# Kernel optimization log

Measured on AMD Instinct MI355X. Metric: run time of the kernel, lower is better.

The kernel has to match this reference:

```python
import jax, jax.numpy as jnp
import numpy as np
import math

H = 8  # num_heads
SCALE = 1.0 / math.sqrt(512.0)  # original divides by sqrt(dim_V), not sqrt(head_dim)


def setup_inputs() -> dict:
    key = jax.random.key(0)
    ks = jax.random.split(key, 16)
    B, N, D = 32, 512, 512
    s = 1.0 / math.sqrt(D)
    return {
        "Q": jax.random.normal(ks[0], (B, N, D), jnp.float32),
        "K": jax.random.normal(ks[1], (B, N, D), jnp.float32),
        "Wq": jax.random.normal(ks[2], (D, D), jnp.float32) * s,
        "bq": jnp.zeros((D,), jnp.float32),
        "Wk": jax.random.normal(ks[3], (D, D), jnp.float32) * s,
        "bk": jnp.zeros((D,), jnp.float32),
        "Wv": jax.random.normal(ks[4], (D, D), jnp.float32) * s,
        "bv": jnp.zeros((D,), jnp.float32),
        "Wo": jax.random.normal(ks[5], (D, D), jnp.float32) * s,
        "bo": jnp.zeros((D,), jnp.float32),
        "W1": jax.random.normal(ks[6], (D, D), jnp.float32) * s,
        "b1": jnp.zeros((D,), jnp.float32),
        "W2": jax.random.normal(ks[7], (D, D), jnp.float32) * s,
        "b2": jnp.zeros((D,), jnp.float32),
    }


def reference(Q, K, Wq, bq, Wk, bk, Wv, bv, Wo, bo, W1, b1, W2, b2):
    B, Nq, D = Q.shape
    dh = D // H
    # projections (torch Linear: x @ W.T + b)
    q = (Q @ Wq.T + bq).reshape(B, Nq, H, dh)
    k = (K @ Wk.T + bk).reshape(B, K.shape[1], H, dh)
    v = (K @ Wv.T + bv).reshape(B, K.shape[1], H, dh)
    # scores: [B, H, Nq, Nk], scaled by 1/sqrt(dim_V)
    scores = jnp.einsum("bqhd,bkhd->bhqk", q, k) * SCALE
    # NOTE: original softmax is over dim=1 of [H*B, Nq, Nk] == the QUERY axis
    A = jax.nn.softmax(scores, axis=2)
    attn = jnp.einsum("bhqk,bkhd->bqhd", A, v).reshape(B, Nq, D)
    out = Q + (attn @ Wo.T + bo)  # dropout p=0.0
    ffn = jax.nn.relu(out @ W1.T + b1) @ W2.T + b2
    return out + ffn
```

## Files before the change

### kernel.cpp

```cpp
#include <hip/hip_runtime.h>
#include <stdint.h>

#define SCALE_ 0.044194173824159216f
#define QSC_ (0.044194173824159216f * 1.4426950408889634f)

typedef __attribute__((ext_vector_type(8))) short bf16x8;
typedef __attribute__((ext_vector_type(4))) float f32x4;
typedef __attribute__((ext_vector_type(16))) float f32x16;
typedef __attribute__((ext_vector_type(2))) unsigned int uint2v;

__device__ __forceinline__ ushort f2b(float f) {
  union { float f; uint32_t u; } v; v.f = f;
  return (ushort)((v.u + 0x7fffu + ((v.u >> 16) & 1u)) >> 16);
}
__device__ __forceinline__ uint32_t cvtpk(float lo, float hi) {
  uint32_t r; asm("v_cvt_pk_bf16_f32 %0, %1, %2" : "=v"(r) : "v"(lo), "v"(hi)); return r;
}
__device__ __forceinline__ float ex2(float x) {
  float r; asm("v_exp_f32 %0, %1" : "=v"(r) : "v"(x)); return r;
}
__device__ __forceinline__ void gld16(void* lds, const void* g) {
  __builtin_amdgcn_global_load_lds(
      (const __attribute__((address_space(1))) uint32_t*)g,
      (__attribute__((address_space(3))) uint32_t*)lds, 16, 0, 0);
}

__global__ __launch_bounds__(256)
void k_cvtw(const float* __restrict__ w0, const float* __restrict__ w1,
            const float* __restrict__ w2, const float* __restrict__ w3,
            const float* __restrict__ w4, const float* __restrict__ w5,
            ushort* __restrict__ Wb)
{
  const int NW = 262144;
  int i = (blockIdx.x * 256 + threadIdx.x) * 4;
  int seg = i >> 18;
  int off = i & (NW - 1);
  const float* src;
  switch (seg) { case 0: src = w0; break; case 1: src = w1; break; case 2: src = w2; break;
                 case 3: src = w3; break; case 4: src = w4; break; default: src = w5; }
  float4 v = *(const float4*)(src + off);
  ushort4 o = make_ushort4(f2b(v.x), f2b(v.y), f2b(v.z), f2b(v.w));
  *(ushort4*)(Wb + (size_t)seg * NW + off) = o;
}

template<int EPI>
__device__ __forceinline__ void gemm_body(const ushort* __restrict__ A, const ushort* __restrict__ Bw,
                                          const float* __restrict__ bias, const float* __restrict__ extra,
                                          float* __restrict__ outf, ushort* __restrict__ outb,
                                          char* lds, int m0, int n0)
{
  const int t = threadIdx.x;
  const int w = t >> 6, lane = t & 63;
  const int wm = w >> 1, wn = w & 1;
  const int rA = lane & 15, g = lane >> 4;

  const ushort* srcA[4]; int ldsA[4];
#pragma unroll
  for (int j = 0; j < 4; j++) {
    int L = (t + j*512) * 16;
    int U = L ^ (((L >> 7) & 7) << 4);
    srcA[j] = A + (size_t)(m0 + (U >> 7))*512 + ((U & 127) >> 1);
    ldsA[j] = L;
  }
  const ushort* srcB[2]; int ldsB[2];
#pragma unroll
  for (int j = 0; j < 2; j++) {
    int L = (t + j*512) * 16;
    int U = L ^ (((L >> 7) & 7) << 4);
    srcB[j] = Bw + (size_t)(n0 + (U >> 7))*512 + ((U & 127) >> 1);
    ldsB[j] = 32768 + L;
  }

#define STAGE_A(ti) do { char* bb_ = lds + ((ti) % 3) * 49152; \
    _Pragma("unroll") \
    for (int j = 0; j < 4; j++) gld16(bb_ + ldsA[j], srcA[j] + (ti)*64); } while (0)
#define STAGE_B(ti) do { char* bb_ = lds + ((ti) % 3) * 49152; \
    _Pragma("unroll") \
    for (int j = 0; j < 2; j++) gld16(bb_ + ldsB[j], srcB[j] + (ti)*64); } while (0)

  STAGE_A(0); STAGE_B(0);
  STAGE_A(1); STAGE_B(1);

  f32x4 acc[4][4] = {};
  for (int i = 0; i < 8; i++) {
    if (i < 7) asm volatile("s_waitcnt vmcnt(6)" ::: "memory");
    else       asm volatile("s_waitcnt vmcnt(0)" ::: "memory");
    __builtin_amdgcn_s_barrier();
    __builtin_amdgcn_sched_barrier(0);
    const char* bufc = lds + (i % 3) * 49152;

    bf16x8 afA[4], bfA[4], afB[4], bfB[4];
#pragma unroll
    for (int m = 0; m < 4; m++) {
      int row = wm*64 + m*16 + rA;
      afA[m] = *(const bf16x8*)(bufc + ((row*128 + g*16) ^ ((row & 7) << 4)));
      afB[m] = *(const bf16x8*)(bufc + ((row*128 + 64 + g*16) ^ ((row & 7) << 4)));
    }
#pragma unroll
    for (int n = 0; n < 4; n++) {
      int row = wn*64 + n*16 + rA;
      bfA[n] = *(const bf16x8*)(bufc + 32768 + ((row*128 + g*16) ^ ((row & 7) << 4)));
      bfB[n] = *(const bf16x8*)(bufc + 32768 + ((row*128 + 64 + g*16) ^ ((row & 7) << 4)));
    }
    if (i < 6) { STAGE_A(i + 2); STAGE_B(i + 2); }
    __builtin_amdgcn_sched_barrier(0);
    __builtin_amdgcn_s_setprio(1);
#pragma unroll
    for (int m = 0; m < 4; m++)
#pragma unroll
      for (int n = 0; n < 4; n++)
        acc[m][n] = __builtin_amdgcn_mfma_f32_16x16x32_bf16(afA[m], bfA[n], acc[m][n], 0, 0, 0);
#pragma unroll
    for (int m = 0; m < 4; m++)
#pragma unroll
      for (int n = 0; n < 4; n++)
        acc[m][n] = __builtin_amdgcn_mfma_f32_16x16x32_bf16(afB[m], bfB[n], acc[m][n], 0, 0, 0);
    __builtin_amdgcn_s_setprio(0);
  }
#undef STAGE_A
#undef STAGE_B

#pragma unroll
  for (int m = 0; m < 4; m++)
#pragma unroll
    for (int n = 0; n < 4; n++) {
      int col = n0 + wn*64 + n*16 + rA;
      float bb = bias[col];
#pragma unroll
      for (int r = 0; r < 4; r++) {
        int row = m0 + wm*64 + m*16 + g*4 + r;
        size_t idx = (size_t)row*512 + col;
        float v = acc[m][n][r] + bb;
        if (EPI == 1)      { float o = extra[idx] + v; outf[idx] = o; outb[idx] = f2b(o); }
        else if (EPI == 2) outb[idx] = f2b(v > 0.f ? v : 0.f);
        else               outf[idx] += v;
      }
    }
}

template<int EPI>
__global__ __launch_bounds__(512, 2)
void k_gemm(const ushort* __restrict__ A, const ushort* __restrict__ Bw,
            const float* __restrict__ bias, const float* __restrict__ extra,
            float* __restrict__ outf, ushort* __restrict__ outb)
{
  __shared__ __align__(16) char lds[3*49152];
  gemm_body<EPI>(A, Bw, bias, extra, outf, outb, lds, blockIdx.x*256, blockIdx.y*128);
}

template<int EPI>
__device__ __forceinline__ void gemm_f32a_body(const float* __restrict__ A32, const ushort* __restrict__ Bw,
                                               const float* __restrict__ bias,
                                               float* __restrict__ outf, ushort* __restrict__ outb,
                                               char* lds, int m0, int n0, float os)
{
  const int t = threadIdx.x;
  const int w = t >> 6, lane = t & 63;
  const int wm = w >> 1, wn = w & 1;
  const int rA = lane & 15, g = lane >> 4;

  const float* srcA[4]; int ldsA[4];
#pragma unroll
  for (int j = 0; j < 4; j++) {
    int L = (t + j*512) * 16;
    int U = L ^ (((L >> 7) & 7) << 4);
    srcA[j] = A32 + (size_t)(m0 + (U >> 7))*512 + ((U & 127) >> 1);
    ldsA[j] = L;
  }
  const ushort* srcB[2]; int ldsB[2];
#pragma unroll
  for (int j = 0; j < 2; j++) {
    int L = (t + j*512) * 16;
    int U = L ^ (((L >> 7) & 7) << 4);
    srcB[j] = Bw + (size_t)(n0 + (U >> 7))*512 + ((U & 127) >> 1);
    ldsB[j] = 32768 + L;
  }

#define QLA(ti, R) do { \
    _Pragma("unroll") \
    for (int j = 0; j < 4; j++) { \
      R[2*j]   = *(const float4*)(srcA[j] + (ti)*64); \
      R[2*j+1] = *(const float4*)(srcA[j] + (ti)*64 + 4); } } while (0)
#define QWA(ti, R) do { char* bb_ = lds + ((ti) % 3) * 49152; \
    _Pragma("unroll") \
    for (int j = 0; j < 4; j++) { \
      uint4 qq; \
      qq.x = cvtpk(R[2*j].x,   R[2*j].y); \
      qq.y = cvtpk(R[2*j].z,   R[2*j].w); \
      qq.z = cvtpk(R[2*j+1].x, R[2*j+1].y); \
      qq.w = cvtpk(R[2*j+1].z, R[2*j+1].w); \
      *(uint4*)(bb_ + ldsA[j]) = qq; } } while (0)
#define QSB(ti) do { char* bb_ = lds + ((ti) % 3) * 49152; \
    _Pragma("unroll") \
    for (int j = 0; j < 2; j++) gld16(bb_ + ldsB[j], srcB[j] + (ti)*64); } while (0)

  float4 a0[8], a1[8];
  QLA(0, a0);
  __builtin_amdgcn_sched_barrier(0);
  QLA(1, a1);
  __builtin_amdgcn_sched_barrier(0);
  QSB(0); QSB(1);
  __builtin_amdgcn_sched_barrier(0);
  asm volatile("s_waitcnt vmcnt(12)" ::: "memory");
  QWA(0, a0);

  f32x4 acc[4][4] = {};

#define QITER(i, RI, RW) do { \
    if ((i) == 0)      asm volatile("s_waitcnt vmcnt(2) lgkmcnt(0)" ::: "memory"); \
    else if ((i) == 7) asm volatile("s_waitcnt vmcnt(0) lgkmcnt(0)" ::: "memory"); \
    else               asm volatile("s_waitcnt vmcnt(10) lgkmcnt(0)" ::: "memory"); \
    __builtin_amdgcn_s_barrier(); \
    __builtin_amdgcn_sched_barrier(0); \
    const char* bufc = lds + ((i) % 3) * 49152; \
    bf16x8 afA[4], bfA[4], afB[4], bfB[4]; \
    _Pragma("unroll") \
    for (int m = 0; m < 4; m++) { \
      int row = wm*64 + m*16 + rA; \
      afA[m] = *(const bf16x8*)(bufc + ((row*128 + g*16) ^ ((row & 7) << 4))); \
      afB[m] = *(const bf16x8*)(bufc + ((row*128 + 64 + g*16) ^ ((row & 7) << 4))); \
    } \
    _Pragma("unroll") \
    for (int n = 0; n < 4; n++) { \
      int row = wn*64 + n*16 + rA; \
      bfA[n] = *(const bf16x8*)(bufc + 32768 + ((row*128 + g*16) ^ ((row & 7) << 4))); \
      bfB[n] = *(const bf16x8*)(bufc + 32768 + ((row*128 + 64 + g*16) ^ ((row & 7) << 4))); \
    } \
    if ((i) < 6) QLA((i) + 2, RI); \
    __builtin_amdgcn_sched_barrier(0); \
    if ((i) < 7) QWA((i) + 1, RW); \
    if ((i) < 6) QSB((i) + 2); \
    __builtin_amdgcn_sched_barrier(0); \
    __builtin_amdgcn_s_setprio(1); \
    _Pragma("unroll") \
    for (int m = 0; m < 4; m++) \
      _Pragma("unroll") \
      for (int n = 0; n < 4; n++) \
        acc[m][n] = __builtin_amdgcn_mfma_f32_16x16x32_bf16(afA[m], bfA[n], acc[m][n], 0, 0, 0); \
    _Pragma("unroll") \
    for (int m = 0; m < 4; m++) \
      _Pragma("unroll") \
      for (int n = 0; n < 4; n++) \
        acc[m][n] = __builtin_amdgcn_mfma_f32_16x16x32_bf16(afB[m], bfB[n], acc[m][n], 0, 0, 0); \
    __builtin_amdgcn_s_setprio(0); \
  } while (0)

  QITER(0, a0, a1);
  QITER(1, a1, a0);
  QITER(2, a0, a1);
  QITER(3, a1, a0);
  QITER(4, a0, a1);
  QITER(5, a1, a0);
  QITER(6, a0, a1);
  QITER(7, a1, a0);
#undef QITER
#undef QLA
#undef QWA
#undef QSB

#pragma unroll
  for (int m = 0; m < 4; m++)
#pragma unroll
    for (int n = 0; n < 4; n++) {
      int col = n0 + wn*64 + n*16 + rA;
      float bb = bias[col];
      if (EPI == 4) {
        int b = m0 >> 9, k0 = m0 & 511;
        int hh = col >> 6, dl = col & 63;
        int kg = k0 + wm*64 + m*16 + g*4;
        float v0 = acc[m][n][0] + bb, v1 = acc[m][n][1] + bb;
        float v2 = acc[m][n][2] + bb, v3 = acc[m][n][3] + bb;
        uint2 pk;
        pk.x = (uint32_t)f2b(v0) | ((uint32_t)f2b(v1) << 16);
        pk.y = (uint32_t)f2b(v2) | ((uint32_t)f2b(v3) << 16);
        *(uint2*)(outb + ((size_t)((b*8 + hh)*64 + dl)*512 + kg)) = pk;
      } else {
#pragma unroll
        for (int r = 0; r < 4; r++) {
          int row = m0 + wm*64 + m*16 + g*4 + r;
          size_t idx = (size_t)row*512 + col;
          outb[idx] = f2b((acc[m][n][r] + bb) * os);
        }
      }
    }
}

__global__ __launch_bounds__(512, 2)
void k_gemm_qkvf(const float* __restrict__ Qf, const float* __restrict__ Kf,
                 const ushort* __restrict__ Wb, const float* __restrict__ bq,
                 const float* __restrict__ bk, const float* __restrict__ bvv,
                 ushort* __restrict__ qkout, ushort* __restrict__ vpT)
{
  __shared__ __align__(16) char lds[3*49152];
  int z = blockIdx.z;
  if (z == 2) {
    gemm_f32a_body<4>(Kf, Wb + 2*(size_t)262144, bvv, nullptr, vpT,
                      lds, blockIdx.x*256, blockIdx.y*128, 1.0f);
  } else if (z == 1) {
    gemm_f32a_body<0>(Kf, Wb + (size_t)262144, bk, nullptr, qkout + (size_t)8388608,
                      lds, blockIdx.x*256, blockIdx.y*128, 1.0f);
  } else {
    gemm_f32a_body<0>(Qf, Wb, bq, nullptr, qkout,
                      lds, blockIdx.x*256, blockIdx.y*128, QSC_);
  }
}

__global__ __launch_bounds__(512, 2)
void k_att2(const ushort* __restrict__ qp, const ushort* __restrict__ kp,
            const ushort* __restrict__ vpT, float* __restrict__ zinv,
            ushort* __restrict__ attn)
{
  __shared__ __align__(16) char kt[65536];
  __shared__ __align__(16) char vt[65536];
  __shared__ __align__(16) char qpr[32768];
  int bh = blockIdx.x;
  int b = bh >> 3, h = bh & 7;
  int t = threadIdx.x, w = t >> 6, lane = t & 63;
  int rA = lane & 15, g = lane >> 4;
  const ushort* kbase = kp + (size_t)(b*512)*512 + h*64;
  const ushort* qbase = qp + (size_t)(b*512)*512 + h*64;
  const ushort* vbase = vpT + (size_t)bh*64*512;

#pragma unroll
  for (int i = 0; i < 8; i++) {
    int c = i*512 + t; int row = c >> 3, sl = c & 7;
    gld16(kt + c*16, kbase + (size_t)row*512 + ((sl ^ (row & 7))*8));
  }
#define STAGE_Q(buf, qb) do { \
    _Pragma("unroll") \
    for (int i = 0; i < 2; i++) { \
      int c = i*512 + t; int row = c >> 3, sl = c & 7; \
      gld16(qpr + (buf)*16384 + c*16, \
            qbase + (size_t)((qb)*128 + row)*512 + ((sl ^ (row & 7))*8)); } } while (0)
  STAGE_Q(0, 0);
  STAGE_Q(1, 1);
#pragma unroll
  for (int i = 0; i < 8; i++) {
    int c = i*512 + t; int d = c >> 6, sl = c & 63;
    gld16(vt + c*16, vbase + (size_t)d*512 + ((sl ^ (d & 7))*8));
  }

  asm volatile("s_waitcnt vmcnt(10)" ::: "memory");
  __builtin_amdgcn_s_barrier();
  __builtin_amdgcn_sched_barrier(0);
  bf16x8 kf[4][2];
#pragma unroll
  for (int n = 0; n < 4; n++)
#pragma unroll
    for (int ks = 0; ks < 2; ks++) {
      int k = w*64 + n*16 + rA;
      kf[n][ks] = *(const bf16x8*)(kt + k*128 + (((ks*4 + g) ^ (k & 7))*16));
    }
  float Zacc[4] = {0.f, 0.f, 0.f, 0.f};
  for (int qb = 0; qb < 4; qb++) {
    if (qb == 1)      { asm volatile("s_waitcnt vmcnt(10)" ::: "memory"); }
    else if (qb == 2) { asm volatile("s_waitcnt vmcnt(2)" ::: "memory"); }
    else if (qb == 3) { asm volatile("s_waitcnt vmcnt(0)" ::: "memory"); }
    if (qb) { __builtin_amdgcn_s_barrier(); __builtin_amdgcn_sched_barrier(0); }
    const char* qtb = qpr + (qb & 1)*16384;
    f32x4 acc[8][4] = {};
#pragma unroll
    for (int ks = 0; ks < 2; ks++) {
      bf16x8 af[8];
#pragma unroll
      for (int m = 0; m < 8; m++) {
        int q = m*16 + rA;
        af[m] = *(const bf16x8*)(qtb + q*128 + (((ks*4 + g) ^ (q & 7))*16));
      }
      __builtin_amdgcn_s_setprio(1);
#pragma unroll
      for (int m = 0; m < 8; m++)
#pragma unroll
        for (int n = 0; n < 4; n++)
          acc[m][n] = __builtin_amdgcn_mfma_f32_16x16x32_bf16(af[m], kf[n][ks], acc[m][n], 0, 0, 0);
      __builtin_amdgcn_s_setprio(0);
    }
    if (qb < 3) __builtin_amdgcn_s_barrier();
    if (qb < 2) STAGE_Q(qb & 1, qb + 2);
#pragma unroll
    for (int m = 0; m < 8; m++)
#pragma unroll
      for (int n = 0; n < 4; n++) {
        float s = 0.f;
#pragma unroll
        for (int r = 0; r < 4; r++) s += ex2(acc[m][n][r]);
        Zacc[n] += s;
      }
  }
#undef STAGE_Q
#pragma unroll
  for (int n = 0; n < 4; n++) {
    float v = Zacc[n];
    v += __shfl_xor(v, 16);
    v += __shfl_xor(v, 32);
    if (lane < 16) ((float*)qpr)[w*64 + n*16 + lane] = 1.0f / v;
  }
  __syncthreads();

  const int l31 = lane & 31, hi5 = lane >> 5;
  bf16x8 qf2[2][4];
#pragma unroll
  for (int qb = 0; qb < 2; qb++)
#pragma unroll
    for (int ksd = 0; ksd < 4; ksd++)
      qf2[qb][ksd] = *(const bf16x8*)(qbase + (size_t)(w*64 + qb*32 + l31)*512 + ksd*16 + hi5*8);
  const float* zl = (const float*)qpr;
  f32x16 oacc[2][2] = {};
  for (int kc = 0; kc < 16; kc++) {
    bf16x8 kf2[4];
#pragma unroll
    for (int ksd = 0; ksd < 4; ksd++) {
      int k = kc*32 + l31;
      kf2[ksd] = *(const bf16x8*)(kt + k*128 + (((ksd*2 + hi5) ^ (k & 7))*16));
    }
    bf16x8 vf2[2][2];
#pragma unroll
    for (int db = 0; db < 2; db++)
#pragma unroll
      for (int ks = 0; ks < 2; ks++) {
        int d = db*32 + l31;
        vf2[db][ks] = *(const bf16x8*)(vt + d*1024 + (((kc*4 + ks*2 + hi5) ^ (d & 7))*16));
      }
    f32x4 zv[4];
#pragma unroll
    for (int j = 0; j < 4; j++)
      zv[j] = *(const f32x4*)(zl + kc*32 + j*8 + hi5*4);
#pragma unroll
    for (int qb = 0; qb < 2; qb++) {
      f32x16 s = {};
      __builtin_amdgcn_s_setprio(1);
#pragma unroll
      for (int ksd = 0; ksd < 4; ksd++)
        s = __builtin_amdgcn_mfma_f32_32x32x16_bf16(kf2[ksd], qf2[qb][ksd], s, 0, 0, 0);
      __builtin_amdgcn_s_setprio(0);
      float e[16];
#pragma unroll
      for (int r = 0; r < 16; r++) e[r] = ex2(s[r]) * zv[r >> 2][r & 3];
      uint32_t x0 = cvtpk(e[0], e[1]),   y0 = cvtpk(e[4], e[5]);
      uint32_t x1 = cvtpk(e[2], e[3]),   y1 = cvtpk(e[6], e[7]);
      uint32_t x2 = cvtpk(e[8], e[9]),   y2 = cvtpk(e[12], e[13]);
      uint32_t x3 = cvtpk(e[10], e[11]), y3 = cvtpk(e[14], e[15]);
      uint2v r0 = __builtin_amdgcn_permlane32_swap(x0, y0, false, false);
      uint2v r1 = __builtin_amdgcn_permlane32_swap(x1, y1, false, false);
      uint2v r2 = __builtin_amdgcn_permlane32_swap(x2, y2, false, false);
      uint2v r3 = __builtin_amdgcn_permlane32_swap(x3, y3, false, false);
      union { uint32_t u[4]; bf16x8 v; } p0, p1;
      p0.u[0] = r0[0]; p0.u[1] = r1[0]; p0.u[2] = r0[1]; p0.u[3] = r1[1];
      p1.u[0] = r2[0]; p1.u[1] = r3[0]; p1.u[2] = r2[1]; p1.u[3] = r3[1];
      __builtin_amdgcn_s_setprio(1);
#pragma unroll
      for (int db = 0; db < 2; db++) {
        oacc[qb][db] = __builtin_amdgcn_mfma_f32_32x32x16_bf16(p0.v, vf2[db][0], oacc[qb][db], 0, 0, 0);
        oacc[qb][db] = __builtin_amdgcn_mfma_f32_32x32x16_bf16(p1.v, vf2[db][1], oacc[qb][db], 0, 0, 0);
      }
      __builtin_amdgcn_s_setprio(0);
    }
  }
#pragma unroll
  for (int qb = 0; qb < 2; qb++)
#pragma unroll
    for (int db = 0; db < 2; db++)
#pragma unroll
      for (int r = 0; r < 16; r++) {
        int q = w*64 + qb*32 + (r & 3) + 8*(r >> 2) + 4*hi5;
        int d = db*32 + l31;
        attn[(size_t)(b*512 + q)*512 + h*64 + d] = f2b(oacc[qb][db][r]);
      }
}

extern "C" void kernel_launch(void* const* d_in, const int* in_sizes, int n_in,
                              void* d_out, int out_size, void* d_ws, size_t ws_size,
                              hipStream_t stream) {
  const float* Q  = (const float*)d_in[0];
  const float* K  = (const float*)d_in[1];
  const float* Wq = (const float*)d_in[2];
  const float* bq = (const float*)d_in[3];
  const float* Wk = (const float*)d_in[4];
  const float* bk = (const float*)d_in[5];
  const float* Wv = (const float*)d_in[6];
  const float* bv = (const float*)d_in[7];
  const float* Wo = (const float*)d_in[8];
  const float* bo = (const float*)d_in[9];
  const float* W1 = (const float*)d_in[10];
  const float* b1 = (const float*)d_in[11];
  const float* W2 = (const float*)d_in[12];
  const float* b2 = (const float*)d_in[13];
  float* out = (float*)d_out;

  const size_t SZ = (size_t)16384 * 512;
  ushort* attn = (ushort*)d_ws;
  ushort* outb = attn + SZ;
  ushort* qp   = outb + SZ;
  ushort* kp   = qp + SZ;
  ushort* vpT  = kp + SZ;
  ushort* Wb   = vpT + SZ;
  float*  zinv = (float*)(Wb + 6 * (size_t)262144);
  ushort* h1   = vpT;

  k_cvtw<<<dim3(1536), dim3(256), 0, stream>>>(Wq, Wk, Wv, Wo, W1, W2, Wb);
  k_gemm_qkvf<<<dim3(64, 4, 3), dim3(512), 0, stream>>>(Q, K, Wb, bq, bk, bv, qp, vpT);
  k_att2<<<dim3(256), dim3(512), 0, stream>>>(qp, kp, vpT, zinv, attn);
  k_gemm<1><<<dim3(64, 4), dim3(512), 0, stream>>>(attn, Wb + 3*(size_t)262144, bo, Q, out, outb);
  k_gemm<2><<<dim3(64, 4), dim3(512), 0, stream>>>(outb, Wb + 4*(size_t)262144, b1, nullptr, nullptr, h1);
  k_gemm<3><<<dim3(64, 4), dim3(512), 0, stream>>>(h1, Wb + 5*(size_t)262144, b2, nullptr, out, nullptr);
}
```

Measured before the change: 146.5 us.

## Deepen Q-projection A-prefetch to three register buffers and split K-half LDS reads

The fp32 A-operand register prefetch in the projection GEMM goes from two to three buffers, so global loads are issued three k-tiles ahead. The bf16 convert-and-write to LDS now happens right after the barrier, ahead of the fragment reads. The second-half LDS fragment reads are moved after the first MFMA batch to overlap with compute and lower live registers. This is meant to hide global load latency better, at the cost of a third 8×float4 register array, which may raise VGPR pressure and hurt occupancy.

New measurement: 146.5 us. Within noise of the previous version (-0.1%).

```diff
diff --git a/kernel.cpp b/kernel.cpp
--- a/kernel.cpp
+++ b/kernel.cpp
@@ -194,41 +194,39 @@
     _Pragma("unroll") \
     for (int j = 0; j < 2; j++) gld16(bb_ + ldsB[j], srcB[j] + (ti)*64); } while (0)
 
-  float4 a0[8], a1[8];
+  float4 a0[8], a1[8], a2[8];
+  QSB(0);
   QLA(0, a0);
+  QLA(1, a1);
+  QLA(2, a2);
+  QSB(1);
   __builtin_amdgcn_sched_barrier(0);
-  QLA(1, a1);
-  __builtin_amdgcn_sched_barrier(0);
-  QSB(0); QSB(1);
-  __builtin_amdgcn_sched_barrier(0);
-  asm volatile("s_waitcnt vmcnt(12)" ::: "memory");
+  asm volatile("s_waitcnt vmcnt(18)" ::: "memory");
   QWA(0, a0);
 
   f32x4 acc[4][4] = {};
 
-#define QITER(i, RI, RW) do { \
-    if ((i) == 0)      asm volatile("s_waitcnt vmcnt(2) lgkmcnt(0)" ::: "memory"); \
-    else if ((i) == 7) asm volatile("s_waitcnt vmcnt(0) lgkmcnt(0)" ::: "memory"); \
-    else               asm volatile("s_waitcnt vmcnt(10) lgkmcnt(0)" ::: "memory"); \
+#define QITER(i, RW, RL) do { \
+    if ((i) <= 5)      asm volatile("s_waitcnt vmcnt(10) lgkmcnt(0)" ::: "memory"); \
+    else if ((i) == 6) asm volatile("s_waitcnt vmcnt(2) lgkmcnt(0)" ::: "memory"); \
+    else               asm volatile("s_waitcnt vmcnt(0) lgkmcnt(0)" ::: "memory"); \
     __builtin_amdgcn_s_barrier(); \
     __builtin_amdgcn_sched_barrier(0); \
+    if ((i) < 7) QWA((i) + 1, RW); \
+    __builtin_amdgcn_sched_barrier(0); \
     const char* bufc = lds + ((i) % 3) * 49152; \
-    bf16x8 afA[4], bfA[4], afB[4], bfB[4]; \
+    bf16x8 afA[4], bfA[4]; \
     _Pragma("unroll") \
     for (int m = 0; m < 4; m++) { \
       int row = wm*64 + m*16 + rA; \
       afA[m] = *(const bf16x8*)(bufc + ((row*128 + g*16) ^ ((row & 7) << 4))); \
-      afB[m] = *(const bf16x8*)(bufc + ((row*128 + 64 + g*16) ^ ((row & 7) << 4))); \
     } \
     _Pragma("unroll") \
     for (int n = 0; n < 4; n++) { \
       int row = wn*64 + n*16 + rA; \
       bfA[n] = *(const bf16x8*)(bufc + 32768 + ((row*128 + g*16) ^ ((row & 7) << 4))); \
-      bfB[n] = *(const bf16x8*)(bufc + 32768 + ((row*128 + 64 + g*16) ^ ((row & 7) << 4))); \
     } \
-    if ((i) < 6) QLA((i) + 2, RI); \
-    __builtin_amdgcn_sched_barrier(0); \
-    if ((i) < 7) QWA((i) + 1, RW); \
+    if ((i) < 5) QLA((i) + 3, RL); \
     if ((i) < 6) QSB((i) + 2); \
     __builtin_amdgcn_sched_barrier(0); \
     __builtin_amdgcn_s_setprio(1); \
@@ -237,6 +235,19 @@
       _Pragma("unroll") \
       for (int n = 0; n < 4; n++) \
         acc[m][n] = __builtin_amdgcn_mfma_f32_16x16x32_bf16(afA[m], bfA[n], acc[m][n], 0, 0, 0); \
+    __builtin_amdgcn_s_setprio(0); \
+    bf16x8 afB[4], bfB[4]; \
+    _Pragma("unroll") \
+    for (int m = 0; m < 4; m++) { \
+      int row = wm*64 + m*16 + rA; \
+      afB[m] = *(const bf16x8*)(bufc + ((row*128 + 64 + g*16) ^ ((row & 7) << 4))); \
+    } \
+    _Pragma("unroll") \
+    for (int n = 0; n < 4; n++) { \
+      int row = wn*64 + n*16 + rA; \
+      bfB[n] = *(const bf16x8*)(bufc + 32768 + ((row*128 + 64 + g*16) ^ ((row & 7) << 4))); \
+    } \
+    __builtin_amdgcn_s_setprio(1); \
     _Pragma("unroll") \
     for (int m = 0; m < 4; m++) \
       _Pragma("unroll") \
@@ -245,14 +256,14 @@
     __builtin_amdgcn_s_setprio(0); \
   } while (0)
 
-  QITER(0, a0, a1);
-  QITER(1, a1, a0);
-  QITER(2, a0, a1);
+  QITER(0, a1, a0);
+  QITER(1, a2, a1);
+  QITER(2, a0, a2);
   QITER(3, a1, a0);
-  QITER(4, a0, a1);
-  QITER(5, a1, a0);
-  QITER(6, a0, a1);
-  QITER(7, a1, a0);
+  QITER(4, a2, a1);
+  QITER(5, a0, a2);
+  QITER(6, a1, a0);
+  QITER(7, a2, a1);
 #undef QITER
 #undef QLA
 #undef QWA
```
